# Performance work log

Hardware: AMD Instinct MI355X
Metric: run time of the kernel (lower is better)

The kernel has to match this reference:

```python
import jax, jax.numpy as jnp
import numpy as np

N_NODES = 50000


def setup_inputs() -> dict:
    key = jax.random.key(0)
    k1, k2, k3, k4, k5 = jax.random.split(key, 5)
    E = 1600000
    features = jax.random.normal(k1, (N_NODES, 256), dtype=jnp.float32)
    weight = jax.random.normal(k2, (256, 64), dtype=jnp.float32) * (1.0 / np.sqrt(256))
    edge_row = jax.random.randint(k3, (E,), 0, N_NODES, dtype=jnp.int64 if jax.config.jax_enable_x64 else jnp.int32)
    edge_col = jax.random.randint(k4, (E,), 0, N_NODES, dtype=jnp.int64 if jax.config.jax_enable_x64 else jnp.int32)
    edge_weight = jax.random.uniform(k5, (E,), dtype=jnp.float32)
    return {
        "features": features,
        "weight": weight,
        "edge_row": edge_row,
        "edge_col": edge_col,
        "edge_weight": edge_weight,
        "active": 1,
    }


def reference(features, weight, edge_row, edge_col, edge_weight, active):
    # support = features @ W  -- dense projection [N, out]
    support = features @ weight
    # output = spmm(adj, support): gather source rows, scale by edge weight,
    # scatter-add into destination rows (COO SpMM).
    msgs = support[edge_col] * edge_weight[:, None]           # [E, out]
    output = jax.ops.segment_sum(msgs, edge_row, num_segments=N_NODES)  # [N, out]
    if active:
        output = jnp.tanh(output)
    return output
```

## Files before the change

### kernel.cpp

```cpp
#include <hip/hip_runtime.h>
#include <hip/hip_fp16.h>
#include <math.h>

#define N_NODES 50000
#define IN_F 256
#define OUT_F 64
#define NBUCK 391
#define CHUNK 4096
#define CAPB 4608

typedef unsigned int uint;
typedef __attribute__((ext_vector_type(8))) short short8v;
typedef __attribute__((ext_vector_type(4))) short short4v;
typedef __attribute__((ext_vector_type(4))) float f32x4;


__device__ __forceinline__ short bf16_trunc(float f) {
    return (short)(__float_as_uint(f) >> 16);
}
__device__ __forceinline__ float bf16_tof(short s) {
    return __uint_as_float(((uint)(unsigned short)s) << 16);
}
__device__ __forceinline__ short bf16_rne(float f) {
    uint u = __float_as_uint(f);
    uint r = u + 0x7FFF + ((u >> 16) & 1);
    return (short)(r >> 16);
}

__global__ __launch_bounds__(256) void wprep_kernel(const float* __restrict__ W,
                                                    short* __restrict__ Whi,
                                                    short* __restrict__ Wlo,
                                                    int* __restrict__ gcnt) {
    const int t = threadIdx.x;
    const int k0 = blockIdx.x * 32;
    if (blockIdx.x == 0) {
        for (int i = t; i < NBUCK; i += 256) gcnt[i] = 0;
    }

    __shared__ float buf[32][65];
    for (int i = t; i < 32 * 64; i += 256) {
        int kk = i >> 6, c = i & 63;
        buf[kk][c] = W[(k0 + kk) * 64 + c];
    }
    __syncthreads();
    {
        int c = t & 63, g = t >> 6;
        short8v vh, vl;
        for (int j = 0; j < 8; ++j) {
            float f = buf[g * 8 + j][c];
            short h = bf16_trunc(f);
            vh[j] = h;
            vl[j] = bf16_rne(f - bf16_tof(h));
        }
        *(short8v*)&Whi[c * IN_F + k0 + g * 8] = vh;
        *(short8v*)&Wlo[c * IN_F + k0 + g * 8] = vl;
    }
}

__global__ __launch_bounds__(256) void gemm_kernel(const float* __restrict__ feat,
                                                   const short* __restrict__ Whi,
                                                   const short* __restrict__ Wlo,
                                                   __half* __restrict__ sup) {
    __shared__ short lds[15360];
    short* As_hi = lds;
    short* As_lo = lds + 5120;
    short* Bs_hi = lds + 10240;
    short* Bs_lo = lds + 12800;

    const int t = threadIdx.x;
    const int row0 = blockIdx.x * 128;
    const int l = t & 63;
    const int lr = l & 15;
    const int lk = (l >> 4) * 8;
    const int wrow = (t >> 6) * 32;

    const int ar = t >> 1, aq = t & 1;
    int gr = row0 + ar; if (gr >= N_NODES) gr = N_NODES - 1;
    const float4* asrc = (const float4*)(feat + (size_t)gr * IN_F);
    const int bc = t >> 2, bp = t & 3;

    f32x4 acc[2][4];
#pragma unroll
    for (int m = 0; m < 2; ++m)
#pragma unroll
        for (int nn = 0; nn < 4; ++nn) acc[m][nn] = (f32x4)(0.f);

    for (int ch = 0; ch < 8; ++ch) {
        float4 av[4];
#pragma unroll
        for (int i = 0; i < 4; ++i) av[i] = asrc[ch * 8 + aq * 4 + i];
        short8v bh = *(const short8v*)(Whi + bc * IN_F + ch * 32 + bp * 8);
        short8v bl = *(const short8v*)(Wlo + bc * IN_F + ch * 32 + bp * 8);

        __syncthreads();
#pragma unroll
        for (int i = 0; i < 4; ++i) {
            float fx[4] = {av[i].x, av[i].y, av[i].z, av[i].w};
            short4v h4, l4;
#pragma unroll
            for (int j = 0; j < 4; ++j) {
                short h = bf16_trunc(fx[j]);
                h4[j] = h;
                l4[j] = bf16_rne(fx[j] - bf16_tof(h));
            }
            *(short4v*)&As_hi[ar * 40 + aq * 16 + i * 4] = h4;
            *(short4v*)&As_lo[ar * 40 + aq * 16 + i * 4] = l4;
        }
        *(short8v*)&Bs_hi[bc * 40 + bp * 8] = bh;
        *(short8v*)&Bs_lo[bc * 40 + bp * 8] = bl;
        __syncthreads();

        short8v ah[2], al[2], wh[4], wl[4];
#pragma unroll
        for (int m = 0; m < 2; ++m) {
            ah[m] = *(short8v*)&As_hi[(wrow + m * 16 + lr) * 40 + lk];
            al[m] = *(short8v*)&As_lo[(wrow + m * 16 + lr) * 40 + lk];
        }
#pragma unroll
        for (int nn = 0; nn < 4; ++nn) {
            wh[nn] = *(short8v*)&Bs_hi[(nn * 16 + lr) * 40 + lk];
            wl[nn] = *(short8v*)&Bs_lo[(nn * 16 + lr) * 40 + lk];
        }
#pragma unroll
        for (int m = 0; m < 2; ++m)
#pragma unroll
            for (int nn = 0; nn < 4; ++nn) {
                acc[m][nn] = __builtin_amdgcn_mfma_f32_16x16x32_bf16(ah[m], wh[nn], acc[m][nn], 0, 0, 0);
                acc[m][nn] = __builtin_amdgcn_mfma_f32_16x16x32_bf16(ah[m], wl[nn], acc[m][nn], 0, 0, 0);
                acc[m][nn] = __builtin_amdgcn_mfma_f32_16x16x32_bf16(al[m], wh[nn], acc[m][nn], 0, 0, 0);
            }
    }

    __syncthreads();
    short* sup_s = lds;
#pragma unroll
    for (int m = 0; m < 2; ++m) {
        int rr = wrow + m * 16 + (l >> 4) * 4;
#pragma unroll
        for (int nn = 0; nn < 4; ++nn) {
            int cc = nn * 16 + lr;
#pragma unroll
            for (int j = 0; j < 4; ++j) {
                __half h = __float2half(acc[m][nn][j]);
                sup_s[(rr + j) * 64 + cc] = *(short*)&h;
            }
        }
    }
    __syncthreads();
    {
        int r = t >> 1, sg = (t & 1) * 32;
        int grow = row0 + r;
        if (grow < N_NODES) {
            const uint4* s4 = (const uint4*)&sup_s[r * 64 + sg];
            uint4* d4 = (uint4*)(sup + (size_t)grow * OUT_F + sg);
            d4[0] = s4[0];
            d4[1] = s4[1];
            d4[2] = s4[2];
            d4[3] = s4[3];
        }
    }
}

__global__ __launch_bounds__(1024) void bin_kernel(const int* __restrict__ erow,
                                                   const int* __restrict__ ecol,
                                                   const float* __restrict__ ew,
                                                   int* __restrict__ gcnt,
                                                   int2* __restrict__ ecw, int E) {
    __shared__ int   h[NBUCK];
    __shared__ uint  pkst[CHUNK];
    __shared__ float wst[CHUNK];
    const int t = threadIdx.x;
    const int base = blockIdx.x * CHUNK;

    for (int i = t; i < NBUCK; i += 1024) h[i] = 0;
    __syncthreads();

    const int e4 = base + 4 * t;
    if (e4 + 3 < E) {
        int4   r4 = *(const int4*)(erow + e4);
        int4   c4 = *(const int4*)(ecol + e4);
        float4 w4 = *(const float4*)(ew + e4);
        pkst[4 * t + 0] = ((uint)r4.x << 16) | (uint)c4.x;
        pkst[4 * t + 1] = ((uint)r4.y << 16) | (uint)c4.y;
        pkst[4 * t + 2] = ((uint)r4.z << 16) | (uint)c4.z;
        pkst[4 * t + 3] = ((uint)r4.w << 16) | (uint)c4.w;
        *(float4*)(wst + 4 * t) = w4;
        atomicAdd(&h[r4.x >> 7], 1);
        atomicAdd(&h[r4.y >> 7], 1);
        atomicAdd(&h[r4.z >> 7], 1);
        atomicAdd(&h[r4.w >> 7], 1);
    } else {
        for (int k = 0; k < 4; ++k) {
            int e = e4 + k;
            if (e < E) {
                int row = erow[e];
                pkst[4 * t + k] = ((uint)row << 16) | (uint)ecol[e];
                wst[4 * t + k] = ew[e];
                atomicAdd(&h[row >> 7], 1);
            }
        }
    }
    __syncthreads();

    for (int i = t; i < NBUCK; i += 1024) {
        int c = h[i];
        if (c > 0) h[i] = atomicAdd(&gcnt[i], c);
    }
    __syncthreads();

    const int lim = min(CHUNK, E - base);
    for (int i = t; i < lim; i += 1024) {
        uint  pk = pkst[i];
        float w  = wst[i];
        int b = (int)(pk >> 23);
        int pos = atomicAdd(&h[b], 1);
        if (pos < CAPB)
            ecw[(size_t)b * CAPB + pos] =
                make_int2((int)(pk & 0x7FFFFF), __float_as_int(w));
    }
}

__global__ __launch_bounds__(512) void reduce_kernel(const __half* __restrict__ sup,
                                                     const int* __restrict__ gcnt,
                                                     const int2* __restrict__ ecw,
                                                     const int* __restrict__ active,
                                                     float* __restrict__ out) {
    __shared__ int2 stB[CAPB];
    __shared__ int h[128];
    __shared__ int sc[128];
    __shared__ int cur[128];
    const int t = threadIdx.x;
    const int b = blockIdx.x;

    int n = gcnt[b]; if (n > CAPB) n = CAPB;
    const int2* eptr = ecw + (size_t)b * CAPB;

    if (t < 128) h[t] = 0;
    __syncthreads();

    for (int i = t; i < n; i += 512) {
        int x = ((const int*)eptr)[2 * i];
        atomicAdd(&h[(x >> 16) & 127], 1);
    }
    __syncthreads();

    if (t < 128) sc[t] = h[t];
    __syncthreads();
    for (int off = 1; off < 128; off <<= 1) {
        int u = (t < 128 && t >= off) ? sc[t - off] : 0;
        __syncthreads();
        if (t < 128) sc[t] += u;
        __syncthreads();
    }
    if (t < 128) cur[t] = sc[t] - h[t];
    __syncthreads();

    for (int i = t; i < n; i += 512) {
        int2 d = eptr[i];
        int r = (d.x >> 16) & 127;
        int pos = atomicAdd(&cur[r], 1);
        stB[pos] = make_int2(d.x & 0xFFFF, d.y);
    }
    __syncthreads();

    const int wid  = t >> 6;
    const int lane = t & 63;
    const int hl   = lane & 31;
    const bool hi  = lane >= 32;
    const int act  = *active;

    for (int r = wid; r < 128; r += 8) {
        int row = b * 128 + r;
        if (row >= N_NODES) break;
        const int s = sc[r] - h[r];
        const int e = sc[r];
        float ax = 0.f, ay = 0.f;
        int j = s;
        for (; j + 8 <= e; j += 8) {
#pragma unroll
            for (int q = 0; q < 4; ++q) {
                int2 pa = stB[j + 2 * q];
                int2 pb = stB[j + 2 * q + 1];
                int   col = hi ? pb.x : pa.x;
                float w   = __int_as_float(hi ? pb.y : pa.y);
                const __half2* hp = (const __half2*)(sup + ((size_t)col << 6));
                float2 v = __half22float2(hp[hl]);
                ax += w * v.x;
                ay += w * v.y;
            }
        }
        for (; j + 2 <= e; j += 2) {
            int2 pa = stB[j];
            int2 pb = stB[j + 1];
            int   col = hi ? pb.x : pa.x;
            float w   = __int_as_float(hi ? pb.y : pa.y);
            const __half2* hp = (const __half2*)(sup + ((size_t)col << 6));
            float2 v = __half22float2(hp[hl]);
            ax += w * v.x;
            ay += w * v.y;
        }
        if (j < e) {
            int2 pa = stB[j];
            int   col = pa.x;
            float w   = hi ? 0.f : __int_as_float(pa.y);
            const __half2* hp = (const __half2*)(sup + ((size_t)col << 6));
            float2 v = __half22float2(hp[hl]);
            ax += w * v.x;
            ay += w * v.y;
        }

        ax += __shfl_xor(ax, 32, 64);
        ay += __shfl_xor(ay, 32, 64);

        if (!hi) {
            if (act) { ax = tanhf(ax); ay = tanhf(ay); }
            *(float2*)&out[((size_t)row << 6) + 2 * hl] = make_float2(ax, ay);
        }
    }
}

extern "C" void kernel_launch(void* const* d_in, const int* in_sizes, int n_in,
                              void* d_out, int out_size, void* d_ws, size_t ws_size,
                              hipStream_t stream) {
    const float* feat = (const float*)d_in[0];
    const float* W    = (const float*)d_in[1];
    const int*   erow = (const int*)d_in[2];
    const int*   ecol = (const int*)d_in[3];
    const float* ew   = (const float*)d_in[4];
    const int*   act  = (const int*)d_in[5];
    float* out = (float*)d_out;

    const int E = in_sizes[2];
    const int G = (E + CHUNK - 1) / CHUNK;

    char* ws = (char*)d_ws;
    __half* sup  = (__half*)ws; ws += (size_t)N_NODES * OUT_F * 2;
    int2*   ecw  = (int2*)ws;   ws += (size_t)NBUCK * CAPB * 8;
    int*    gcnt = (int*)ws;    ws += ((size_t)NBUCK * 4 + 15) & ~15;
    short*  Whi  = (short*)ws;  ws += (size_t)OUT_F * IN_F * 2;
    short*  Wlo  = (short*)ws;  ws += (size_t)OUT_F * IN_F * 2;

    wprep_kernel<<<8, 256, 0, stream>>>(W, Whi, Wlo, gcnt);
    gemm_kernel<<<(N_NODES + 127) / 128, 256, 0, stream>>>(feat, Whi, Wlo, sup);
    bin_kernel<<<G, 1024, 0, stream>>>(erow, ecol, ew, gcnt, ecw, E);
    reduce_kernel<<<NBUCK, 512, 0, stream>>>(sup, gcnt, ecw, act, out);
}
```

Baseline: 188.9 us.

## Replace per-row CSR sort in reduce with fixed-point LDS atomic accumulation

The reduce kernel drops the per-bucket histogram, prefix scan and counting sort of edges by destination row. It now streams edge chunks into shared memory and has each wave atomically add fixed-point scaled messages into a 128x64 integer accumulator held in LDS, converting back to float before tanh. This removes several sync-heavy passes and the sorted staging buffer. In exchange it issues one LDS atomic per edge per feature lane, loads half-precision values one per lane instead of two, and adds fixed-point quantization error that could overflow for large sums.

```diff
diff --git a/kernel.cpp b/kernel.cpp
--- a/kernel.cpp
+++ b/kernel.cpp
@@ -8,6 +8,7 @@
 #define NBUCK 391
 #define CHUNK 4096
 #define CAPB 4608
+#define RCHK 1024
 
 typedef unsigned int uint;
 typedef __attribute__((ext_vector_type(8))) short short8v;
@@ -225,96 +226,66 @@
                                                      const int2* __restrict__ ecw,
                                                      const int* __restrict__ active,
                                                      float* __restrict__ out) {
-    __shared__ int2 stB[CAPB];
-    __shared__ int h[128];
-    __shared__ int sc[128];
-    __shared__ int cur[128];
+    __shared__ int  acc[128 * 64];
+    __shared__ int2 meta[RCHK];
     const int t = threadIdx.x;
     const int b = blockIdx.x;
+    const int wid  = t >> 6;
+    const int lane = t & 63;
+    const float SCALE = 1048576.0f;
+    const float INV   = 9.5367431640625e-7f;
+
+    for (int i = t; i < 2048; i += 512)
+        ((int4*)acc)[i] = make_int4(0, 0, 0, 0);
 
     int n = gcnt[b]; if (n > CAPB) n = CAPB;
     const int2* eptr = ecw + (size_t)b * CAPB;
 
-    if (t < 128) h[t] = 0;
-    __syncthreads();
-
-    for (int i = t; i < n; i += 512) {
-        int x = ((const int*)eptr)[2 * i];
-        atomicAdd(&h[(x >> 16) & 127], 1);
-    }
-    __syncthreads();
-
-    if (t < 128) sc[t] = h[t];
-    __syncthreads();
-    for (int off = 1; off < 128; off <<= 1) {
-        int u = (t < 128 && t >= off) ? sc[t - off] : 0;
+    for (int c0 = 0; c0 < n; c0 += RCHK) {
+        const int m = min(RCHK, n - c0);
         __syncthreads();
-        if (t < 128) sc[t] += u;
+        for (int i = t; i < m; i += 512) meta[i] = eptr[c0 + i];
         __syncthreads();
-    }
-    if (t < 128) cur[t] = sc[t] - h[t];
-    __syncthreads();
-
-    for (int i = t; i < n; i += 512) {
-        int2 d = eptr[i];
-        int r = (d.x >> 16) & 127;
-        int pos = atomicAdd(&cur[r], 1);
-        stB[pos] = make_int2(d.x & 0xFFFF, d.y);
-    }
-    __syncthreads();
-
-    const int wid  = t >> 6;
-    const int lane = t & 63;
-    const int hl   = lane & 31;
-    const bool hi  = lane >= 32;
-    const int act  = *active;
-
-    for (int r = wid; r < 128; r += 8) {
+
+        for (int e = wid * 4; e < m; e += 32) {
+            if (e + 4 <= m) {
+                int2 d0 = meta[e + 0];
+                int2 d1 = meta[e + 1];
+                int2 d2 = meta[e + 2];
+                int2 d3 = meta[e + 3];
+                float v0 = __half2float(sup[(size_t)((d0.x & 0xFFFF) << 6) + lane]);
+                float v1 = __half2float(sup[(size_t)((d1.x & 0xFFFF) << 6) + lane]);
+                float v2 = __half2float(sup[(size_t)((d2.x & 0xFFFF) << 6) + lane]);
+                float v3 = __half2float(sup[(size_t)((d3.x & 0xFFFF) << 6) + lane]);
+                float s0 = __int_as_float(d0.y) * SCALE;
+                float s1 = __int_as_float(d1.y) * SCALE;
+                float s2 = __int_as_float(d2.y) * SCALE;
+                float s3 = __int_as_float(d3.y) * SCALE;
+                atomicAdd(&acc[(((d0.x >> 16) & 127) << 6) + lane], (int)(v0 * s0));
+                atomicAdd(&acc[(((d1.x >> 16) & 127) << 6) + lane], (int)(v1 * s1));
+                atomicAdd(&acc[(((d2.x >> 16) & 127) << 6) + lane], (int)(v2 * s2));
+                atomicAdd(&acc[(((d3.x >> 16) & 127) << 6) + lane], (int)(v3 * s3));
+            } else {
+                for (int k = e; k < m; ++k) {
+                    int2 d = meta[k];
+                    float v = __half2float(sup[(size_t)((d.x & 0xFFFF) << 6) + lane]);
+                    float s = __int_as_float(d.y) * SCALE;
+                    atomicAdd(&acc[(((d.x >> 16) & 127) << 6) + lane], (int)(v * s));
+                }
+            }
+        }
+    }
+    __syncthreads();
+
+    const int act = *active;
+    for (int i = t; i < 2048; i += 512) {
+        int r = i >> 4;
         int row = b * 128 + r;
-        if (row >= N_NODES) break;
-        const int s = sc[r] - h[r];
-        const int e = sc[r];
-        float ax = 0.f, ay = 0.f;
-        int j = s;
-        for (; j + 8 <= e; j += 8) {
-#pragma unroll
-            for (int q = 0; q < 4; ++q) {
-                int2 pa = stB[j + 2 * q];
-                int2 pb = stB[j + 2 * q + 1];
-                int   col = hi ? pb.x : pa.x;
-                float w   = __int_as_float(hi ? pb.y : pa.y);
-                const __half2* hp = (const __half2*)(sup + ((size_t)col << 6));
-                float2 v = __half22float2(hp[hl]);
-                ax += w * v.x;
-                ay += w * v.y;
-            }
-        }
-        for (; j + 2 <= e; j += 2) {
-            int2 pa = stB[j];
-            int2 pb = stB[j + 1];
-            int   col = hi ? pb.x : pa.x;
-            float w   = __int_as_float(hi ? pb.y : pa.y);
-            const __half2* hp = (const __half2*)(sup + ((size_t)col << 6));
-            float2 v = __half22float2(hp[hl]);
-            ax += w * v.x;
-            ay += w * v.y;
-        }
-        if (j < e) {
-            int2 pa = stB[j];
-            int   col = pa.x;
-            float w   = hi ? 0.f : __int_as_float(pa.y);
-            const __half2* hp = (const __half2*)(sup + ((size_t)col << 6));
-            float2 v = __half22float2(hp[hl]);
-            ax += w * v.x;
-            ay += w * v.y;
-        }
-
-        ax += __shfl_xor(ax, 32, 64);
-        ay += __shfl_xor(ay, 32, 64);
-
-        if (!hi) {
-            if (act) { ax = tanhf(ax); ay = tanhf(ay); }
-            *(float2*)&out[((size_t)row << 6) + 2 * hl] = make_float2(ax, ay);
+        if (row < N_NODES) {
+            int4 q = ((const int4*)acc)[i];
+            float4 v = make_float4(q.x * INV, q.y * INV, q.z * INV, q.w * INV);
+            if (act) { v.x = tanhf(v.x); v.y = tanhf(v.y); v.z = tanhf(v.z); v.w = tanhf(v.w); }
+            *(float4*)&out[((size_t)row << 6) + (i & 15) * 4] = v;
         }
     }
 }
```

Result: slower. 206.8 us (+9.5%).
